# Kernel optimization log

Hardware: AMD Instinct MI355X
Metric: run time of the kernel (lower is better)

Reference implementation:

```python
import jax, jax.numpy as jnp
import numpy as np

BLOCK_SIZE = 256
N_EMBD = 768
HEAD_SIZE = 768  # == n_embd so RoPE table (dim=n_embd) matches channel pairing


def _rope_tables(T, dim, theta0=10000.0):
    # compute_freq(dim=n_embd, seq_len=block_size, theta_0=10000):
    # theta_j = theta0^(-2j/dim), angle[t, j] = t * theta_j
    j = jnp.arange(dim // 2, dtype=jnp.float32)
    theta = jnp.float32(theta0) ** (-2.0 * j / jnp.float32(dim))
    ang = jnp.arange(T, dtype=jnp.float32)[:, None] * theta[None, :]  # [T, dim/2]
    return jnp.cos(ang), jnp.sin(ang)


def _apply_rope(t, cos, sin):
    # t: [B, T, D]; pair adjacent channels (2j, 2j+1) as complex, rotate.
    B, T, D = t.shape
    tr = t.reshape(B, T, D // 2, 2)
    re, im = tr[..., 0], tr[..., 1]
    out_re = re * cos[None] - im * sin[None]
    out_im = re * sin[None] + im * cos[None]
    return jnp.stack([out_re, out_im], axis=-1).reshape(B, T, D)


def setup_inputs() -> dict:
    key = jax.random.key(0)
    k1, k2, k3, k4 = jax.random.split(key, 4)
    B, T = 128, BLOCK_SIZE
    x = jax.random.normal(k1, (B, T, N_EMBD), dtype=jnp.float32)
    Wq = jax.random.normal(k2, (N_EMBD, HEAD_SIZE), dtype=jnp.float32) * 0.02
    Wk = jax.random.normal(k3, (N_EMBD, HEAD_SIZE), dtype=jnp.float32) * 0.02
    Wv = jax.random.normal(k4, (N_EMBD, HEAD_SIZE), dtype=jnp.float32) * 0.02
    return {"x": x, "Wq": Wq, "Wk": Wk, "Wv": Wv}


def reference(x, Wq, Wk, Wv):
    B, T, C = x.shape
    q = x @ Wq  # [B, T, D]
    k = x @ Wk
    v = x @ Wv
    cos, sin = _rope_tables(T, HEAD_SIZE)
    q = _apply_rope(q, cos, sin)
    k = _apply_rope(k, cos, sin)
    scale = jnp.float32(HEAD_SIZE) ** -0.5
    wei = jnp.einsum('bqd,bkd->bqk', q, k) * scale  # [B, T, T]
    causal = jnp.tril(jnp.ones((T, T), dtype=bool))
    wei = jnp.where(causal[None], wei, -jnp.inf)
    wei = jax.nn.softmax(wei, axis=-1)
    # dropout(p=0.2) is identity in eval/deterministic baseline
    out = jnp.einsum('bqk,bkd->bqd', wei, v)  # [B, T, D]
    return out
```

## Files before the change

### kernel.cpp

```cpp
#include <hip/hip_runtime.h>
#include <hip/hip_bf16.h>
#include <stdint.h>


typedef __attribute__((ext_vector_type(8))) short short8;
typedef __attribute__((ext_vector_type(4))) short short4v;
typedef __attribute__((ext_vector_type(4))) float f32x4;

__device__ __forceinline__ short f2bf(float f) {
    uint32_t u = __float_as_uint(f);
    u += 0x7fffu + ((u >> 16) & 1u);
    return (short)(u >> 16);
}

__global__ __launch_bounds__(256) void cvt_x(const float* __restrict__ x,
                                             short* __restrict__ xb) {
    long i = ((long)blockIdx.x * 256 + threadIdx.x) * 4;
    f32x4 v = *(const f32x4*)(x + i);
    short4v o;
    o.x = f2bf(v.x); o.y = f2bf(v.y); o.z = f2bf(v.z); o.w = f2bf(v.w);
    *(short4v*)(xb + i) = o;
}

__global__ __launch_bounds__(256) void cvt_wt(const float* __restrict__ W,
                                              short* __restrict__ Wt) {
    __shared__ float tile[32][33];
    int d0 = blockIdx.x * 32, c0 = blockIdx.y * 32;
    int tr = threadIdx.x >> 5, tc = threadIdx.x & 31;
    #pragma unroll
    for (int i = 0; i < 32; i += 8)
        tile[tr + i][tc] = W[(long)(c0 + tr + i) * 768 + d0 + tc];
    __syncthreads();
    #pragma unroll
    for (int i = 0; i < 32; i += 8)
        Wt[(long)(d0 + tr + i) * 768 + c0 + tc] = f2bf(tile[tc][tr + i]);
}

__global__ __launch_bounds__(256) void rope_tab(float2* __restrict__ rt) {
    int i = blockIdx.x * 256 + threadIdx.x;
    int t = i / 384, j = i - t * 384;
    const float CE = -0.034603417655f;
    float th = exp2f((float)j * CE);
    float s, c;
    sincosf((float)t * th, &s, &c);
    rt[i] = make_float2(c, s);
}

template <int EPI, int CAUSAL>
__global__ __launch_bounds__(256)
void gemm_bt(const short* __restrict__ A, const short* __restrict__ B,
             void* __restrict__ C, void* __restrict__ C2, void* __restrict__ C3,
             const float2* __restrict__ rt,
             int M, int N, int K, long sA, long sB, long sC, float scale) {
    __shared__ short lA[128 * 32];
    __shared__ short lB[128 * 32];
    const int m0 = blockIdx.y * 128;
    const int n0 = blockIdx.x * 128;
    if (CAUSAL == 1 && n0 > m0) return;
    const int bz = blockIdx.z;
    const short* Ab = A + (long)bz * sA;
    const short* Bb = B + (long)bz * sB;
    const int tid = threadIdx.x;
    const int w = tid >> 6, lane = tid & 63;
    const int wm = (w >> 1) * 64;
    const int wn = (w & 1) * 64;
    const int lrow = lane >> 2;
    const int lcol = ((((lane & 3) - (lrow >> 1)) & 3)) * 8;
    const int sw8 = (((lane >> 4) + ((lane & 15) >> 1)) & 3) * 8;

    const int Kend = (CAUSAL == 2) ? (m0 + 128 < K ? m0 + 128 : K) : K;

    f32x4 acc[4][4] = {};

    for (int k0 = 0; k0 < Kend; k0 += 32) {
        #pragma unroll
        for (int c2 = 0; c2 < 2; ++c2) {
            int seg = c2 * 4 + w;
            int row = seg * 16 + lrow;
            const short* ga = Ab + (long)(m0 + row) * K + k0 + lcol;
            __builtin_amdgcn_global_load_lds(
                (const __attribute__((address_space(1))) void*)ga,
                (__attribute__((address_space(3))) void*)(lA + seg * 512),
                16, 0, 0);
            const short* gb = Bb + (long)(n0 + row) * K + k0 + lcol;
            __builtin_amdgcn_global_load_lds(
                (const __attribute__((address_space(1))) void*)gb,
                (__attribute__((address_space(3))) void*)(lB + seg * 512),
                16, 0, 0);
        }
        __syncthreads();

        short8 af[4], bfr[4];
        const int ar = wm + (lane & 15);
        const int br = wn + (lane & 15);
        #pragma unroll
        for (int tmi = 0; tmi < 4; ++tmi)
            af[tmi] = *(const short8*)(lA + (ar + tmi * 16) * 32 + sw8);
        #pragma unroll
        for (int tni = 0; tni < 4; ++tni)
            bfr[tni] = *(const short8*)(lB + (br + tni * 16) * 32 + sw8);
        #pragma unroll
        for (int tmi = 0; tmi < 4; ++tmi)
            #pragma unroll
            for (int tni = 0; tni < 4; ++tni)
                acc[tmi][tni] = __builtin_amdgcn_mfma_f32_16x16x32_bf16(
                    af[tmi], bfr[tni], acc[tmi][tni], 0, 0, 0);
        __syncthreads();
    }

    const int r0 = wm + (lane >> 4) * 4;
    const int c0 = wn + (lane & 15);

    if (EPI == 2) {
        #pragma unroll
        for (int tmi = 0; tmi < 4; ++tmi)
            #pragma unroll
            for (int tni = 0; tni < 4; ++tni)
                #pragma unroll
                for (int r = 0; r < 4; ++r) {
                    int row = m0 + r0 + tmi * 16 + r;
                    int col = n0 + c0 + tni * 16;
                    ((float*)C)[(long)bz * sC + (long)row * N + col] =
                        acc[tmi][tni][r] * scale;
                }
    } else {
        const int type = (n0 >= 1536) ? 2 : (n0 >= 768 ? 1 : 0);
        const int nl0 = n0 - type * 768;
        if (type < 2) {
            short* dst = (type == 0) ? (short*)C : (short*)C2;
            const int par = lane & 1;
            #pragma unroll
            for (int tmi = 0; tmi < 4; ++tmi)
                #pragma unroll
                for (int tni = 0; tni < 4; ++tni) {
                    int col = nl0 + c0 + tni * 16;
                    const float2* rtc = rt + (col >> 1);
                    #pragma unroll
                    for (int r = 0; r < 4; ++r) {
                        int row = m0 + r0 + tmi * 16 + r;
                        float val = acc[tmi][tni][r];
                        float pv = __shfl_xor(val, 1);
                        float2 cs = rtc[(row & 255) * 384];
                        float re = par ? pv : val;
                        float im = par ? val : pv;
                        float o = par ? (re * cs.y + im * cs.x)
                                      : (re * cs.x - im * cs.y);
                        dst[(long)row * 768 + col] = f2bf(o);
                    }
                }
        } else {
            short* vt = (short*)C3;
            #pragma unroll
            for (int tmi = 0; tmi < 4; ++tmi)
                #pragma unroll
                for (int tni = 0; tni < 4; ++tni) {
                    int col = nl0 + c0 + tni * 16;
                    #pragma unroll
                    for (int r = 0; r < 4; ++r) {
                        int row = m0 + r0 + tmi * 16 + r;
                        vt[((long)(row >> 8) * 768 + col) * 256 + (row & 255)] =
                            f2bf(acc[tmi][tni][r]);
                    }
                }
        }
    }
}

__global__ __launch_bounds__(256) void softmax_p(const float* __restrict__ S,
                                                 short* __restrict__ P) {
    int wv = threadIdx.x >> 6, lane = threadIdx.x & 63;
    int row = blockIdx.x * 4 + wv;
    int t = row & 255;
    f32x4 v = *(const f32x4*)(S + (long)row * 256 + lane * 4);
    float vals[4];
    float m = -1e30f;
    #pragma unroll
    for (int j = 0; j < 4; ++j) {
        int n = lane * 4 + j;
        vals[j] = (n <= t) ? v[j] : -1e30f;
        m = fmaxf(m, vals[j]);
    }
    #pragma unroll
    for (int o = 32; o; o >>= 1) m = fmaxf(m, __shfl_xor(m, o));
    float e[4], sum = 0.f;
    #pragma unroll
    for (int j = 0; j < 4; ++j) { e[j] = __expf(vals[j] - m); sum += e[j]; }
    #pragma unroll
    for (int o = 32; o; o >>= 1) sum += __shfl_xor(sum, o);
    float inv = 1.0f / sum;
    short4v o4;
    o4.x = f2bf(e[0] * inv); o4.y = f2bf(e[1] * inv);
    o4.z = f2bf(e[2] * inv); o4.w = f2bf(e[3] * inv);
    *(short4v*)(P + (long)row * 256 + lane * 4) = o4;
}

extern "C" void kernel_launch(void* const* d_in, const int* in_sizes, int n_in,
                              void* d_out, int out_size, void* d_ws, size_t ws_size,
                              hipStream_t stream) {
    const float* x  = (const float*)d_in[0];
    const float* Wq = (const float*)d_in[1];
    const float* Wk = (const float*)d_in[2];
    const float* Wv = (const float*)d_in[3];

    char* ws = (char*)d_ws;
    short*  xb = (short*)(ws);
    short*  wt = (short*)(ws + 50331648);
    short*  qb = (short*)(ws + 53870592);
    short*  kb = (short*)(ws + 104202240);
    short*  vt = (short*)(ws + 154533888);
    float*  S  = (float*)(ws + 204865536);
    short*  P  = (short*)(ws + 238419968);
    float2* rt = (float2*)(ws + 255197184);

    cvt_x<<<24576, 256, 0, stream>>>(x, xb);
    dim3 gw(24, 24);
    cvt_wt<<<gw, 256, 0, stream>>>(Wq, wt);
    cvt_wt<<<gw, 256, 0, stream>>>(Wk, wt + 589824);
    cvt_wt<<<gw, 256, 0, stream>>>(Wv, wt + 1179648);
    rope_tab<<<384, 256, 0, stream>>>(rt);

    dim3 g1(18, 256, 1);
    gemm_bt<3, 0><<<g1, 256, 0, stream>>>(xb, wt, qb, kb, vt, rt,
                                          32768, 2304, 768, 0, 0, 0, 1.0f);

    dim3 g2(2, 2, 128);
    gemm_bt<2, 1><<<g2, 256, 0, stream>>>(qb, kb, S, nullptr, nullptr, nullptr,
                                          256, 256, 768, 196608, 196608, 65536,
                                          0.0360843918f);

    softmax_p<<<8192, 256, 0, stream>>>(S, P);

    dim3 g3(6, 2, 128);
    gemm_bt<2, 2><<<g3, 256, 0, stream>>>(P, vt, (float*)d_out, nullptr, nullptr,
                                          nullptr, 256, 768, 256, 65536, 196608,
                                          196608, 1.0f);
}
```

Before: 463.6 us.

## Double GEMM K-tile to 64 and remap blocks for XCD-aware L2 locality

The GEMM kernel now stages a 64-wide K slice per iteration instead of 32, with a new 8-way XOR swizzle for LDS loads and reads. This halves the number of barrier pairs per output tile and doubles the MFMA work between syncs. Each launch also gets a block-index remapping that groups blocks sharing A rows or batch entries onto the same XCD (p&7), so they can reuse data through that XCD's L2. LDS use doubles to 32KB per block, which could reduce occupancy.

```diff
diff --git a/kernel.cpp b/kernel.cpp
--- a/kernel.cpp
+++ b/kernel.cpp
@@ -46,37 +46,59 @@
     rt[i] = make_float2(c, s);
 }
 
-template <int EPI, int CAUSAL>
+template <int EPI, int CAUSAL, int SWZ>
 __global__ __launch_bounds__(256)
 void gemm_bt(const short* __restrict__ A, const short* __restrict__ B,
              void* __restrict__ C, void* __restrict__ C2, void* __restrict__ C3,
              const float2* __restrict__ rt,
              int M, int N, int K, long sA, long sB, long sC, float scale) {
-    __shared__ short lA[128 * 32];
-    __shared__ short lB[128 * 32];
-    const int m0 = blockIdx.y * 128;
-    const int n0 = blockIdx.x * 128;
+    int bx, by, bz;
+    if (SWZ == 1) {
+        int p = blockIdx.x + 18 * blockIdx.y;
+        int c = p & 7, j = p >> 3;
+        int st = j / 18;
+        by = c * 32 + st; bx = j - st * 18; bz = 0;
+    } else if (SWZ == 2) {
+        int p = blockIdx.x + 2 * (blockIdx.y + 2 * blockIdx.z);
+        int c = p & 7, j = p >> 3;
+        bz = c * 16 + (j >> 2);
+        by = (j >> 1) & 1; bx = j & 1;
+    } else if (SWZ == 3) {
+        int p = blockIdx.x + 6 * (blockIdx.y + 2 * blockIdx.z);
+        int c = p & 7, j = p >> 3;
+        int bt = j / 12;
+        bz = c * 16 + bt;
+        int t = j - bt * 12;
+        by = t / 6; bx = t - (t / 6) * 6;
+    } else {
+        bx = blockIdx.x; by = blockIdx.y; bz = blockIdx.z;
+    }
+    const int m0 = by * 128;
+    const int n0 = bx * 128;
     if (CAUSAL == 1 && n0 > m0) return;
-    const int bz = blockIdx.z;
+
+    __shared__ short lA[128 * 64];
+    __shared__ short lB[128 * 64];
     const short* Ab = A + (long)bz * sA;
     const short* Bb = B + (long)bz * sB;
     const int tid = threadIdx.x;
     const int w = tid >> 6, lane = tid & 63;
     const int wm = (w >> 1) * 64;
     const int wn = (w & 1) * 64;
-    const int lrow = lane >> 2;
-    const int lcol = ((((lane & 3) - (lrow >> 1)) & 3)) * 8;
-    const int sw8 = (((lane >> 4) + ((lane & 15) >> 1)) & 3) * 8;
+    const int lrow8 = lane >> 3;
+    const int lcol = (((lane & 7) - lrow8) & 7) * 8;
+    const int fr = lane & 15;
+    const int kq = lane >> 4;
 
     const int Kend = (CAUSAL == 2) ? (m0 + 128 < K ? m0 + 128 : K) : K;
 
     f32x4 acc[4][4] = {};
 
-    for (int k0 = 0; k0 < Kend; k0 += 32) {
+    for (int k0 = 0; k0 < Kend; k0 += 64) {
         #pragma unroll
-        for (int c2 = 0; c2 < 2; ++c2) {
-            int seg = c2 * 4 + w;
-            int row = seg * 16 + lrow;
+        for (int i = 0; i < 4; ++i) {
+            int seg = i * 4 + w;
+            int row = seg * 8 + lrow8;
             const short* ga = Ab + (long)(m0 + row) * K + k0 + lcol;
             __builtin_amdgcn_global_load_lds(
                 (const __attribute__((address_space(1))) void*)ga,
@@ -90,21 +112,23 @@
         }
         __syncthreads();
 
-        short8 af[4], bfr[4];
-        const int ar = wm + (lane & 15);
-        const int br = wn + (lane & 15);
         #pragma unroll
-        for (int tmi = 0; tmi < 4; ++tmi)
-            af[tmi] = *(const short8*)(lA + (ar + tmi * 16) * 32 + sw8);
-        #pragma unroll
-        for (int tni = 0; tni < 4; ++tni)
-            bfr[tni] = *(const short8*)(lB + (br + tni * 16) * 32 + sw8);
-        #pragma unroll
-        for (int tmi = 0; tmi < 4; ++tmi)
+        for (int c = 0; c < 2; ++c) {
+            const int sphys = ((c * 4 + kq + fr) & 7) * 8;
+            short8 af[4], bfr[4];
+            #pragma unroll
+            for (int tmi = 0; tmi < 4; ++tmi)
+                af[tmi] = *(const short8*)(lA + (wm + fr + tmi * 16) * 64 + sphys);
             #pragma unroll
             for (int tni = 0; tni < 4; ++tni)
-                acc[tmi][tni] = __builtin_amdgcn_mfma_f32_16x16x32_bf16(
-                    af[tmi], bfr[tni], acc[tmi][tni], 0, 0, 0);
+                bfr[tni] = *(const short8*)(lB + (wn + fr + tni * 16) * 64 + sphys);
+            #pragma unroll
+            for (int tmi = 0; tmi < 4; ++tmi)
+                #pragma unroll
+                for (int tni = 0; tni < 4; ++tni)
+                    acc[tmi][tni] = __builtin_amdgcn_mfma_f32_16x16x32_bf16(
+                        af[tmi], bfr[tni], acc[tmi][tni], 0, 0, 0);
+        }
         __syncthreads();
     }
 
@@ -220,18 +244,18 @@
     rope_tab<<<384, 256, 0, stream>>>(rt);
 
     dim3 g1(18, 256, 1);
-    gemm_bt<3, 0><<<g1, 256, 0, stream>>>(xb, wt, qb, kb, vt, rt,
-                                          32768, 2304, 768, 0, 0, 0, 1.0f);
+    gemm_bt<3, 0, 1><<<g1, 256, 0, stream>>>(xb, wt, qb, kb, vt, rt,
+                                             32768, 2304, 768, 0, 0, 0, 1.0f);
 
     dim3 g2(2, 2, 128);
-    gemm_bt<2, 1><<<g2, 256, 0, stream>>>(qb, kb, S, nullptr, nullptr, nullptr,
-                                          256, 256, 768, 196608, 196608, 65536,
-                                          0.0360843918f);
+    gemm_bt<2, 1, 2><<<g2, 256, 0, stream>>>(qb, kb, S, nullptr, nullptr, nullptr,
+                                             256, 256, 768, 196608, 196608, 65536,
+                                             0.0360843918f);
 
     softmax_p<<<8192, 256, 0, stream>>>(S, P);
 
     dim3 g3(6, 2, 128);
-    gemm_bt<2, 2><<<g3, 256, 0, stream>>>(P, vt, (float*)d_out, nullptr, nullptr,
-                                          nullptr, 256, 768, 256, 65536, 196608,
-                                          196608, 1.0f);
-}
+    gemm_bt<2, 2, 3><<<g3, 256, 0, stream>>>(P, vt, (float*)d_out, nullptr,
+                                             nullptr, nullptr, 256, 768, 256,
+                                             65536, 196608, 196608, 1.0f);
+}
```

Result: faster. 449.5 us (-3.1%).
